# Kernel optimization log

Hardware: AMD Instinct MI355X
Metric: run time of the kernel (lower is better)

## Reference

```python
import jax, jax.numpy as jnp
import numpy as np

STATE_DIM = 28224  # 84*84*4 flattened Atari stack
N_EPISODE = 8192
FEATURE_DIM = 32
K_NEAREST = 10
C = 0.001
EPS_KERNEL = 0.001


def setup_inputs() -> dict:
    key = jax.random.key(0)
    ks = jax.random.split(key, 5)
    s = jax.random.normal(ks[0], (1, STATE_DIM), dtype=jnp.float32)
    episode = jax.random.normal(ks[1], (N_EPISODE, STATE_DIM), dtype=jnp.float32)
    dm2 = jnp.ones((1,), dtype=jnp.float32)  # running distance stat (torch inits 0.0; 1.0 avoids div-by-zero)
    # fan-in scaled weights so activations stay O(1)
    W1 = jax.random.normal(ks[2], (STATE_DIM, 128), dtype=jnp.float32) / np.sqrt(STATE_DIM)
    b1 = jnp.zeros((128,), dtype=jnp.float32)
    W2 = jax.random.normal(ks[3], (128, 64), dtype=jnp.float32) / np.sqrt(128.0)
    b2 = jnp.zeros((64,), dtype=jnp.float32)
    W3 = jax.random.normal(ks[4], (64, FEATURE_DIM), dtype=jnp.float32) / np.sqrt(64.0)
    b3 = jnp.zeros((FEATURE_DIM,), dtype=jnp.float32)
    return {"s": s, "episode": episode, "dm2": dm2,
            "W1": W1, "b1": b1, "W2": W2, "b2": b2, "W3": W3, "b3": b3}


def _embed(x, W1, b1, W2, b2, W3, b3):
    h = jax.nn.relu(x @ W1 + b1)
    h = jax.nn.relu(h @ W2 + b2)
    return h @ W3 + b3  # [*, FEATURE_DIM]


def reference(s, episode, dm2, W1, b1, W2, b2, W3, b3):
    z_s = _embed(s, W1, b1, W2, b2, W3, b3)          # [1, F]
    z_ep = _embed(episode, W1, b1, W2, b2, W3, b3)   # [N, F]
    dist = jnp.linalg.norm(z_s - z_ep, axis=1)       # [N]
    kernel = EPS_KERNEL / (dist / dm2[0] + EPS_KERNEL)
    top_k_kernel, _ = jax.lax.top_k(kernel, K_NEAREST)           # largest kernel values
    neg_top_dist, _ = jax.lax.top_k(-dist, K_NEAREST)            # smallest distances
    top_k_dist = -neg_top_dist
    new_dm2 = 0.99 * dm2[0] + 0.01 * jnp.mean(top_k_dist)        # running-stat update
    reward_episodic = 1.0 / (jnp.sqrt(jnp.mean(top_k_kernel)) + C)
    return reward_episodic, new_dm2
```

## Files before the change

### kernel.cpp

```cpp
#include <hip/hip_runtime.h>
#include <hip/hip_bf16.h>

typedef __attribute__((ext_vector_type(8))) __bf16 bf16x8;
typedef __attribute__((ext_vector_type(4))) float f32x4;
typedef __attribute__((ext_vector_type(4))) unsigned short u16x4;

#define STATE_DIM 28224
#define NEP 8192
#define MPAD 8320
#define KSPLIT 7
#define KSTEPS 63
#define BK 64
#define NWG (65 * KSPLIT)
#define EPSK 0.001f
#define CC 0.001f

#define WT_BYTES   (441 * 8192 * 2)
#define PART_BYTES (KSPLIT * MPAD * 128 * 2)
#define DIST_BYTES (NEP * 4)
#define WS_NEEDED  (WT_BYTES + PART_BYTES + DIST_BYTES)

__device__ __forceinline__ unsigned short f2bf(float f) {
    unsigned int u = __float_as_uint(f);
    u += 0x7fffu + ((u >> 16) & 1u);
    return (unsigned short)(u >> 16);
}

__device__ __forceinline__ void glds16(const void* g, void* l) {
    __builtin_amdgcn_global_load_lds(
        (const __attribute__((address_space(1))) unsigned int*)g,
        (__attribute__((address_space(3))) unsigned int*)l, 16, 0, 0);
}

__global__ __launch_bounds__(256) void prep_wt(const float* __restrict__ W1,
                                               unsigned short* __restrict__ WtS) {
    __shared__ __align__(16) unsigned short img[8192];
    const int c = blockIdx.x;
    const int tid = threadIdx.x;
    const int k0 = c * 64;
#pragma unroll
    for (int i = 0; i < 32; ++i) {
        const int f = i * 256 + tid;
        const int k = f >> 7, n = f & 127;
        const float wv = W1[(size_t)(k0 + k) * 128 + n];
        const int ad = ((n * 128 + k * 2) ^ ((n & 7) << 4)) >> 1;
        img[ad] = f2bf(wv);
    }
    __syncthreads();
    unsigned short* dst = WtS + (size_t)c * 8192;
#pragma unroll
    for (int i = 0; i < 4; ++i) {
        const int f = i * 256 + tid;
        *reinterpret_cast<uint4*>(dst + f * 8) =
            *reinterpret_cast<const uint4*>(img + f * 8);
    }
}

__global__ __launch_bounds__(256, 2) void gemm1(const float* __restrict__ ep,
                                                const float* __restrict__ s,
                                                const unsigned short* __restrict__ WtS,
                                                unsigned short* __restrict__ part) {
    __shared__ __align__(16) unsigned char smA[128 * 64 * 2];
    __shared__ __align__(16) unsigned char smB[2][128 * 64 * 2];

    const int hw = blockIdx.x;
    const int xcd = hw & 7, slot = hw >> 3;
    const int q = NWG >> 3, r = NWG & 7;
    const int bid = (xcd < r ? xcd * (q + 1) : r * (q + 1) + (xcd - r) * q) + slot;

    const int ks = bid / 65;
    const int mt = bid % 65;
    const int tid = threadIdx.x;
    const int kBase = ks * (KSTEPS * BK);
    const int chunkBase = ks * KSTEPS;

    const int mBase = tid >> 4;
    const int kOff = (tid & 15) * 4;
    const int swzW = (mBase & 7) << 4;

    const bool last = (mt == 64);
    const int rowBase = mt * 128;

    float4 aR[8];

    auto loadA = [&](int kc) {
#pragma unroll
        for (int i = 0; i < 8; ++i) {
            const int m = mBase + i * 16;
            const int rg = rowBase + m;
            if (!last) {
                aR[i] = *reinterpret_cast<const float4*>(ep + (size_t)rg * STATE_DIM + kc + kOff);
            } else {
                if (rg < NEP)
                    aR[i] = *reinterpret_cast<const float4*>(ep + (size_t)rg * STATE_DIM + kc + kOff);
                else if (rg == NEP)
                    aR[i] = *reinterpret_cast<const float4*>(s + kc + kOff);
                else
                    aR[i] = make_float4(0.f, 0.f, 0.f, 0.f);
            }
        }
    };

    const int w = tid >> 6;
    const int lane = tid & 63;

    auto stageB = [&](int chunkIdx, int buf) {
        const char* cb = (const char*)(WtS + (size_t)chunkIdx * 8192);
#pragma unroll
        for (int r2 = 0; r2 < 4; ++r2) {
            const int off = ((r2 << 2) + w) << 10;
            glds16(cb + off + (lane << 4), &smB[buf][off]);
        }
    };

    auto writeLdsA = [&]() {
#pragma unroll
        for (int i = 0; i < 8; ++i) {
            const int m = mBase + i * 16;
            u16x4 av;
            av[0] = f2bf(aR[i].x); av[1] = f2bf(aR[i].y);
            av[2] = f2bf(aR[i].z); av[3] = f2bf(aR[i].w);
            const int ad = (m * 128 + kOff * 2) ^ swzW;
            *reinterpret_cast<u16x4*>(smA + ad) = av;
        }
    };

    const int wr = w >> 1, wc = w & 1;
    const int l15 = lane & 15, lq = lane >> 4;
    const int swzF = (l15 & 7) << 4;

    f32x4 acc[4][4] = {};

    auto compute = [&](int buf) {
#pragma unroll
        for (int kh = 0; kh < 2; ++kh) {
            bf16x8 af[4], bf[4];
#pragma unroll
            for (int mf = 0; mf < 4; ++mf) {
                const int row = wr * 64 + mf * 16 + l15;
                const int ad = (row * 128 + (kh * 32 + lq * 8) * 2) ^ swzF;
                af[mf] = *reinterpret_cast<const bf16x8*>(smA + ad);
            }
#pragma unroll
            for (int nf = 0; nf < 4; ++nf) {
                const int row = wc * 64 + nf * 16 + l15;
                const int ad = (row * 128 + (kh * 32 + lq * 8) * 2) ^ swzF;
                bf[nf] = *reinterpret_cast<const bf16x8*>(smB[buf] + ad);
            }
#pragma unroll
            for (int mf = 0; mf < 4; ++mf)
#pragma unroll
                for (int nf = 0; nf < 4; ++nf)
                    acc[mf][nf] = __builtin_amdgcn_mfma_f32_16x16x32_bf16(
                        af[mf], bf[nf], acc[mf][nf], 0, 0, 0);
        }
    };

    loadA(kBase);
    stageB(chunkBase, 0);
    int buf = 0;
    for (int t2 = 0; t2 < KSTEPS; ++t2) {
        __syncthreads();
        writeLdsA();
        __syncthreads();
        if (t2 + 1 < KSTEPS) {
            loadA(kBase + (t2 + 1) * BK);
            stageB(chunkBase + t2 + 1, buf ^ 1);
        }
        compute(buf);
        buf ^= 1;
    }

    unsigned short* po = part + ((size_t)ks * MPAD + rowBase) * 128;
#pragma unroll
    for (int mf = 0; mf < 4; ++mf)
#pragma unroll
        for (int nf = 0; nf < 4; ++nf)
#pragma unroll
            for (int v = 0; v < 4; ++v) {
                const int row = wr * 64 + mf * 16 + lq * 4 + v;
                const int col = wc * 64 + nf * 16 + l15;
                po[(size_t)row * 128 + col] = f2bf(acc[mf][nf][v]);
            }
}

__global__ __launch_bounds__(256) void mlp23(const unsigned short* __restrict__ part,
                                             const float* __restrict__ b1,
                                             const float* __restrict__ W2,
                                             const float* __restrict__ b2,
                                             const float* __restrict__ W3,
                                             const float* __restrict__ b3,
                                             float* __restrict__ dist) {
    __shared__ float W2t[64 * 129];
    __shared__ float W3t[32 * 65];
    __shared__ float b1L[128], b2L[64], b3L[32];
    __shared__ float h1buf[4][128];
    __shared__ float h2buf[4][64];
    __shared__ float zsL[32];

    const int tid = threadIdx.x;
#pragma unroll
    for (int i = 0; i < 32; ++i) {
        int f = tid + i * 256;
        W2t[(f & 63) * 129 + (f >> 6)] = W2[f];
    }
#pragma unroll
    for (int i = 0; i < 8; ++i) {
        int f = tid + i * 256;
        W3t[(f & 31) * 65 + (f >> 5)] = W3[f];
    }
    if (tid < 128) b1L[tid] = b1[tid];
    if (tid < 64) b2L[tid] = b2[tid];
    if (tid < 32) b3L[tid] = b3[tid];
    __syncthreads();

    const unsigned int* pu = (const unsigned int*)part;
    const int w = tid >> 6, l = tid & 63;

    if (w == 0) {
        float h1a = b1L[2 * l], h1b = b1L[2 * l + 1];
#pragma unroll
        for (int p = 0; p < KSPLIT; ++p) {
            const unsigned int u = pu[((size_t)p * MPAD + NEP) * 64 + l];
            h1a += __uint_as_float(u << 16);
            h1b += __uint_as_float(u & 0xffff0000u);
        }
        *reinterpret_cast<float2*>(&h1buf[0][2 * l]) =
            make_float2(fmaxf(h1a, 0.f), fmaxf(h1b, 0.f));
        float s0 = 0.f, s1 = 0.f, s2 = 0.f, s3 = 0.f;
        const float* wr2 = &W2t[l * 129];
        const float* hb = h1buf[0];
#pragma unroll 8
        for (int k = 0; k < 32; ++k) {
            s0 += hb[k]      * wr2[k];
            s1 += hb[k + 32] * wr2[k + 32];
            s2 += hb[k + 64] * wr2[k + 64];
            s3 += hb[k + 96] * wr2[k + 96];
        }
        h2buf[0][l] = fmaxf(b2L[l] + ((s0 + s1) + (s2 + s3)), 0.f);
        const int c = l & 31;
        const float* wr3 = &W3t[c * 65];
        const float* h2 = h2buf[0];
        float t0 = 0.f, t1 = 0.f;
#pragma unroll 8
        for (int k = 0; k < 32; ++k) {
            t0 += h2[k]      * wr3[k];
            t1 += h2[k + 32] * wr3[k + 32];
        }
        if (l < 32) zsL[c] = b3L[c] + t0 + t1;
    }
    __syncthreads();

    const int base = blockIdx.x * 16 + w * 4;
    for (int rr = 0; rr < 4; ++rr) {
        const int r = base + rr;
        float h1a = b1L[2 * l], h1b = b1L[2 * l + 1];
#pragma unroll
        for (int p = 0; p < KSPLIT; ++p) {
            const unsigned int u = pu[((size_t)p * MPAD + r) * 64 + l];
            h1a += __uint_as_float(u << 16);
            h1b += __uint_as_float(u & 0xffff0000u);
        }
        h1a = fmaxf(h1a, 0.f);
        h1b = fmaxf(h1b, 0.f);
        *reinterpret_cast<float2*>(&h1buf[w][2 * l]) = make_float2(h1a, h1b);
        float s0 = 0.f, s1 = 0.f, s2 = 0.f, s3 = 0.f;
        const float* wr2 = &W2t[l * 129];
        const float* hb = h1buf[w];
#pragma unroll 8
        for (int k = 0; k < 32; ++k) {
            s0 += hb[k]      * wr2[k];
            s1 += hb[k + 32] * wr2[k + 32];
            s2 += hb[k + 64] * wr2[k + 64];
            s3 += hb[k + 96] * wr2[k + 96];
        }
        float a2 = fmaxf(b2L[l] + ((s0 + s1) + (s2 + s3)), 0.f);
        h2buf[w][l] = a2;
        const int c = l & 31;
        const float* wr3 = &W3t[c * 65];
        const float* h2 = h2buf[w];
        float t0 = 0.f, t1 = 0.f;
#pragma unroll 8
        for (int k = 0; k < 32; ++k) {
            t0 += h2[k]      * wr3[k];
            t1 += h2[k + 32] * wr3[k + 32];
        }
        const float zc = b3L[c] + t0 + t1;
        const float d = zc - zsL[c];
        float d2 = d * d;
#pragma unroll
        for (int sft = 1; sft < 32; sft <<= 1)
            d2 += __shfl_xor(d2, sft);
        if (l == 0) dist[r] = sqrtf(d2);
    }
}

__global__ __launch_bounds__(256) void top10_k(const float* __restrict__ dist,
                                               const float* __restrict__ dm2,
                                               float* __restrict__ out) {
    const int t = threadIdx.x;
    float v[32];
#pragma unroll
    for (int i = 0; i < 32; ++i) v[i] = dist[i * 256 + t];

    __shared__ float wv[4];
    __shared__ int wi[4];

    const float dm = dm2[0];
    float sd = 0.f, sk = 0.f;

    for (int round = 0; round < 10; ++round) {
        float bv = 3.0e38f;
        int bi = 0x7fffffff;
#pragma unroll
        for (int i = 0; i < 32; ++i) {
            const float x = v[i];
            const int idx = i * 256 + t;
            if (x < bv) { bv = x; bi = idx; }
        }
#pragma unroll
        for (int sft = 1; sft < 64; sft <<= 1) {
            const float ov = __shfl_xor(bv, sft);
            const int oi = __shfl_xor(bi, sft);
            if (ov < bv || (ov == bv && oi < bi)) { bv = ov; bi = oi; }
        }
        const int wid = t >> 6;
        if ((t & 63) == 0) { wv[wid] = bv; wi[wid] = bi; }
        __syncthreads();
        bv = wv[0]; bi = wi[0];
#pragma unroll
        for (int k = 1; k < 4; ++k) {
            const float ov = wv[k]; const int oi = wi[k];
            if (ov < bv || (ov == bv && oi < bi)) { bv = ov; bi = oi; }
        }
        __syncthreads();
#pragma unroll
        for (int i = 0; i < 32; ++i)
            if (bi == i * 256 + t) v[i] = 3.0e38f;
        sd += bv;
        sk += EPSK / (bv / dm + EPSK);
    }

    if (t == 0) {
        const float meand = sd * 0.1f;
        const float meank = sk * 0.1f;
        out[0] = 1.0f / (sqrtf(meank) + CC);
        out[1] = 0.99f * dm + 0.01f * meand;
    }
}

extern "C" void kernel_launch(void* const* d_in, const int* in_sizes, int n_in,
                              void* d_out, int out_size, void* d_ws, size_t ws_size,
                              hipStream_t stream) {
    const float* s   = (const float*)d_in[0];
    const float* ep  = (const float*)d_in[1];
    const float* dm2 = (const float*)d_in[2];
    const float* W1  = (const float*)d_in[3];
    const float* b1  = (const float*)d_in[4];
    const float* W2  = (const float*)d_in[5];
    const float* b2  = (const float*)d_in[6];
    const float* W3  = (const float*)d_in[7];
    const float* b3  = (const float*)d_in[8];
    float* out = (float*)d_out;

    if (ws_size < (size_t)WS_NEEDED) return;

    unsigned short* WtS  = (unsigned short*)d_ws;
    unsigned short* part = (unsigned short*)((char*)d_ws + WT_BYTES);
    float* dist = (float*)((char*)d_ws + WT_BYTES + PART_BYTES);

    hipLaunchKernelGGL(prep_wt, dim3(441), dim3(256), 0, stream, W1, WtS);
    hipLaunchKernelGGL(gemm1, dim3(NWG), dim3(256), 0, stream, ep, s, WtS, part);
    hipLaunchKernelGGL(mlp23, dim3(512), dim3(256), 0, stream, part, b1, W2, b2, W3, b3, dist);
    hipLaunchKernelGGL(top10_k, dim3(1), dim3(256), 0, stream, dist, dm2, out);
}
```

Baseline: 228.1 us.

## Move query row out of GEMM tiles and rebalance split-K to 512 workgroups

The single query row s is now projected by a separate small fp32 kernel that writes its W1 partials directly. This lets the main GEMM drop the padded 65th M-tile and its branchy loads. The split-K grid is reshaped to 64 M-tiles by 8 K-splits (55 steps each, 56 for the last), giving 512 workgroups that map evenly onto the 256 CUs at two per CU. The cost is an extra kernel launch and a slightly uneven last K-split. The s row also keeps fp32 inputs instead of bf16, which changes numerics slightly.

```diff
diff --git a/kernel.cpp b/kernel.cpp
--- a/kernel.cpp
+++ b/kernel.cpp
@@ -7,16 +7,18 @@
 
 #define STATE_DIM 28224
 #define NEP 8192
-#define MPAD 8320
-#define KSPLIT 7
-#define KSTEPS 63
+#define PROWS 8256
+#define KSPLIT 8
+#define NMT 64
+#define NWG (NMT * KSPLIT)
 #define BK 64
-#define NWG (65 * KSPLIT)
 #define EPSK 0.001f
 #define CC 0.001f
 
+#define KSTEP_BASE 55
+
 #define WT_BYTES   (441 * 8192 * 2)
-#define PART_BYTES (KSPLIT * MPAD * 128 * 2)
+#define PART_BYTES (KSPLIT * PROWS * 128 * 2)
 #define DIST_BYTES (NEP * 4)
 #define WS_NEEDED  (WT_BYTES + PART_BYTES + DIST_BYTES)
 
@@ -56,29 +58,47 @@
     }
 }
 
+__global__ __launch_bounds__(256) void srow_k(const float* __restrict__ s,
+                                              const float* __restrict__ W1,
+                                              unsigned short* __restrict__ part) {
+    __shared__ float red[128];
+    const int b = blockIdx.x;
+    const int t = threadIdx.x;
+    const int col = t & 127, kh = t >> 7;
+    const int k0 = b * 3528 + kh * 1764;
+    float a0 = 0.f, a1 = 0.f, a2 = 0.f, a3 = 0.f;
+    for (int k = 0; k < 1764; k += 4) {
+        a0 += s[k0 + k]     * W1[(size_t)(k0 + k)     * 128 + col];
+        a1 += s[k0 + k + 1] * W1[(size_t)(k0 + k + 1) * 128 + col];
+        a2 += s[k0 + k + 2] * W1[(size_t)(k0 + k + 2) * 128 + col];
+        a3 += s[k0 + k + 3] * W1[(size_t)(k0 + k + 3) * 128 + col];
+    }
+    const float acc = (a0 + a1) + (a2 + a3);
+    if (kh == 1) red[col] = acc;
+    __syncthreads();
+    if (kh == 0)
+        part[((size_t)b * PROWS + NEP) * 128 + col] = f2bf(acc + red[col]);
+}
+
 __global__ __launch_bounds__(256, 2) void gemm1(const float* __restrict__ ep,
-                                                const float* __restrict__ s,
                                                 const unsigned short* __restrict__ WtS,
                                                 unsigned short* __restrict__ part) {
     __shared__ __align__(16) unsigned char smA[128 * 64 * 2];
     __shared__ __align__(16) unsigned char smB[2][128 * 64 * 2];
 
     const int hw = blockIdx.x;
-    const int xcd = hw & 7, slot = hw >> 3;
-    const int q = NWG >> 3, r = NWG & 7;
-    const int bid = (xcd < r ? xcd * (q + 1) : r * (q + 1) + (xcd - r) * q) + slot;
-
-    const int ks = bid / 65;
-    const int mt = bid % 65;
+    const int bid = (hw & 7) * 64 + (hw >> 3);
+    const int ks = bid >> 6;
+    const int mt = bid & 63;
     const int tid = threadIdx.x;
-    const int kBase = ks * (KSTEPS * BK);
-    const int chunkBase = ks * KSTEPS;
+
+    const int nsteps = KSTEP_BASE + (ks == 7);
+    const int kBase = ks * (KSTEP_BASE * BK);
+    const int chunkBase = ks * KSTEP_BASE;
 
     const int mBase = tid >> 4;
     const int kOff = (tid & 15) * 4;
     const int swzW = (mBase & 7) << 4;
-
-    const bool last = (mt == 64);
     const int rowBase = mt * 128;
 
     float4 aR[8];
@@ -86,18 +106,8 @@
     auto loadA = [&](int kc) {
 #pragma unroll
         for (int i = 0; i < 8; ++i) {
-            const int m = mBase + i * 16;
-            const int rg = rowBase + m;
-            if (!last) {
-                aR[i] = *reinterpret_cast<const float4*>(ep + (size_t)rg * STATE_DIM + kc + kOff);
-            } else {
-                if (rg < NEP)
-                    aR[i] = *reinterpret_cast<const float4*>(ep + (size_t)rg * STATE_DIM + kc + kOff);
-                else if (rg == NEP)
-                    aR[i] = *reinterpret_cast<const float4*>(s + kc + kOff);
-                else
-                    aR[i] = make_float4(0.f, 0.f, 0.f, 0.f);
-            }
+            const int rg = rowBase + mBase + i * 16;
+            aR[i] = *reinterpret_cast<const float4*>(ep + (size_t)rg * STATE_DIM + kc + kOff);
         }
     };
 
@@ -159,11 +169,11 @@
     loadA(kBase);
     stageB(chunkBase, 0);
     int buf = 0;
-    for (int t2 = 0; t2 < KSTEPS; ++t2) {
+    for (int t2 = 0; t2 < nsteps; ++t2) {
         __syncthreads();
         writeLdsA();
         __syncthreads();
-        if (t2 + 1 < KSTEPS) {
+        if (t2 + 1 < nsteps) {
             loadA(kBase + (t2 + 1) * BK);
             stageB(chunkBase + t2 + 1, buf ^ 1);
         }
@@ -171,7 +181,7 @@
         buf ^= 1;
     }
 
-    unsigned short* po = part + ((size_t)ks * MPAD + rowBase) * 128;
+    unsigned short* po = part + ((size_t)ks * PROWS + rowBase) * 128;
 #pragma unroll
     for (int mf = 0; mf < 4; ++mf)
 #pragma unroll
@@ -221,7 +231,7 @@
         float h1a = b1L[2 * l], h1b = b1L[2 * l + 1];
 #pragma unroll
         for (int p = 0; p < KSPLIT; ++p) {
-            const unsigned int u = pu[((size_t)p * MPAD + NEP) * 64 + l];
+            const unsigned int u = pu[((size_t)p * PROWS + NEP) * 64 + l];
             h1a += __uint_as_float(u << 16);
             h1b += __uint_as_float(u & 0xffff0000u);
         }
@@ -257,7 +267,7 @@
         float h1a = b1L[2 * l], h1b = b1L[2 * l + 1];
 #pragma unroll
         for (int p = 0; p < KSPLIT; ++p) {
-            const unsigned int u = pu[((size_t)p * MPAD + r) * 64 + l];
+            const unsigned int u = pu[((size_t)p * PROWS + r) * 64 + l];
             h1a += __uint_as_float(u << 16);
             h1b += __uint_as_float(u & 0xffff0000u);
         }
@@ -370,7 +380,8 @@
     float* dist = (float*)((char*)d_ws + WT_BYTES + PART_BYTES);
 
     hipLaunchKernelGGL(prep_wt, dim3(441), dim3(256), 0, stream, W1, WtS);
-    hipLaunchKernelGGL(gemm1, dim3(NWG), dim3(256), 0, stream, ep, s, WtS, part);
+    hipLaunchKernelGGL(srow_k, dim3(8), dim3(256), 0, stream, s, W1, part);
+    hipLaunchKernelGGL(gemm1, dim3(NWG), dim3(256), 0, stream, ep, WtS, part);
     hipLaunchKernelGGL(mlp23, dim3(512), dim3(256), 0, stream, part, b1, W2, b2, W3, b3, dist);
     hipLaunchKernelGGL(top10_k, dim3(1), dim3(256), 0, stream, dist, dm2, out);
 }
```

New measurement: 300.8 us. 1.32x slower.
